# Kernel tuning notes

Measured on AMD Instinct MI355X. Metric: run time of the kernel, lower is better.

The kernel has to match this reference:

```python
import jax, jax.numpy as jnp
import numpy as np

D = 300  # feature dim hardcoded in the layer
L = 50   # headline length (e = ones(50))
B = 16384


def setup_inputs() -> dict:
    key = jax.random.key(0)
    ks = jax.random.split(key, 7)
    s = 0.05  # keras initializations.get('normal') uses scale=0.05
    return {
        "Y": jax.random.normal(ks[0], (B, D, L), dtype=jnp.float32),
        "h_n": jax.random.normal(ks[1], (B, D), dtype=jnp.float32),
        "W_y": s * jax.random.normal(ks[2], (D, D), dtype=jnp.float32),
        "W_h": s * jax.random.normal(ks[3], (D, D), dtype=jnp.float32),
        "W_p": s * jax.random.normal(ks[4], (D, D), dtype=jnp.float32),
        "W_x": s * jax.random.normal(ks[5], (D, D), dtype=jnp.float32),
        "w": s * jax.random.normal(ks[6], (D,), dtype=jnp.float32),
    }


def reference(Y, h_n, W_y, W_h, W_p, W_x, w):
    # M = tanh(W_y Y + (W_h h_n) e^T)   -> [B, D, L]
    Wh_h = jnp.einsum('de,be->bd', W_h, h_n)            # [B, D]
    M = jnp.tanh(jnp.einsum('de,bel->bdl', W_y, Y) + Wh_h[:, :, None])
    # alpha = softmax(w^T M) over headline positions    -> [B, L]
    alpha = jax.nn.softmax(jnp.einsum('d,bdl->bl', w, M), axis=-1)
    # r = Y alpha^T                                      -> [B, D]
    r = jnp.einsum('bdl,bl->bd', Y, alpha)
    # h* = tanh(W_p r + W_x h_n)                         -> [B, D]
    h = jnp.tanh(jnp.einsum('de,be->bd', W_p, r) + jnp.einsum('de,be->bd', W_x, h_n))
    return h
```

## Files before the change

### kernel.cpp

```cpp
#include <hip/hip_runtime.h>
#include <hip/hip_bf16.h>

typedef __attribute__((ext_vector_type(8))) short bf16x8;
typedef __attribute__((ext_vector_type(4))) float f32x4;
typedef unsigned short u16;
typedef unsigned int u32;

__device__ __forceinline__ u16 f2bf(float f){
    u32 u; __builtin_memcpy(&u,&f,4);
    u = (u + 0x7FFFu + ((u>>16)&1u)) >> 16;
    return (u16)u;
}
__device__ __forceinline__ float bf2f(u16 h){
    u32 u = ((u32)h)<<16; float f; __builtin_memcpy(&f,&u,4); return f;
}
__device__ __forceinline__ u32 pkbf(float a, float b){
    __hip_bfloat162 h = __float22bfloat162_rn(float2{a,b});
    u32 r; __builtin_memcpy(&r,&h,4); return r;
}
__device__ __forceinline__ float fast_tanh(float x){
    float e = __builtin_amdgcn_exp2f(x * 2.8853900817779268f);
    return 1.f - 2.f*__builtin_amdgcn_rcpf(e + 1.f);
}
__device__ __forceinline__ float wval(const float* W, int d, int e){
    return (d<300 && e<300) ? W[d*300+e] : 0.f;
}
__device__ __forceinline__ int yslot(int row){
    return (((row&15) ^ ((row>>2)&3) ^ ((row&48)>>2))) << 4;
}

__global__ void k_prep(const float* __restrict__ Wy, const float* __restrict__ Wh,
                       const float* __restrict__ Wp, const float* __restrict__ Wx,
                       const float* __restrict__ w,
                       u16* __restrict__ wy_swz, u16* __restrict__ wh_swz,
                       u16* __restrict__ wpx_swz, float* __restrict__ w_pad)
{
    int gid = blockIdx.x*256 + threadIdx.x;
    if (gid < 320) w_pad[gid] = (gid < 300) ? w[gid] : 0.f;
    u16* dst; const float* A; const float* Bm = nullptr; int t, nks;
    if (gid < 12800)      { dst = wy_swz;  t = gid;        nks = 10; A = Wy; }
    else if (gid < 25600) { dst = wh_swz;  t = gid-12800;  nks = 10; A = Wh; }
    else                  { dst = wpx_swz; t = gid-25600;  nks = 20; A = Wp; Bm = Wx; }
    int ks   = (t/64) % nks;
    int tile = t/(nks*64);
    int lane = t & 63;
    int d  = tile*16 + (lane & 15);
    int kb = ks*32 + (lane>>4)*8;
    u32 pk[4];
    #pragma unroll
    for (int jj=0; jj<4; jj++){
        int k0 = kb + 2*jj, k1 = k0 + 1;
        float v0, v1;
        if (Bm){ v0 = (k0 < 320) ? wval(A,d,k0) : wval(Bm,d,k0-320);
                 v1 = (k1 < 320) ? wval(A,d,k1) : wval(Bm,d,k1-320); }
        else   { v0 = wval(A,d,k0); v1 = wval(A,d,k1); }
        pk[jj] = (u32)f2bf(v0) | ((u32)f2bf(v1) << 16);
    }
    uint4 u; u.x = pk[0]; u.y = pk[1]; u.z = pk[2]; u.w = pk[3];
    ((uint4*)dst)[t] = u;
}

__global__ __launch_bounds__(256,3) void k_whh(const float* __restrict__ hn,
        const u16* __restrict__ wh_swz, u16* __restrict__ whh)
{
    __shared__ __align__(16) u16 A[64*328];
    int tid = threadIdx.x;
    int rb = blockIdx.x >> 1, half = blockIdx.x & 1;
    int m0 = rb*64;
    for (int i = tid; i < 9600; i += 256){
        int r = i/150, c = (i%150)*2;
        float2 v = *(const float2*)(hn + (size_t)(m0+r)*300 + c);
        *(u32*)&A[r*328 + c] = pkbf(v.x, v.y);
    }
    for (int i = tid; i < 64*14; i += 256){ int r = i/14, c = 300 + (i%14)*2; *(u32*)&A[r*328+c] = 0; }
    __syncthreads();
    int w = tid>>6, lane = tid&63, lo = lane&15, hi = lane>>4;
    f32x4 acc[10];
    #pragma unroll
    for (int t=0; t<10; t++) acc[t] = (f32x4){0.f,0.f,0.f,0.f};
    const bf16x8* wsz = (const bf16x8*)wh_swz;
    for (int ks=0; ks<10; ks++){
        bf16x8 aF = *(const bf16x8*)&A[(w*16+lo)*328 + ks*32 + hi*8];
        #pragma unroll
        for (int t=0; t<10; t++){
            int nt = half*10 + t;
            bf16x8 bF = wsz[(nt*10+ks)*64 + lane];
            acc[t] = __builtin_amdgcn_mfma_f32_16x16x32_bf16(aF, bF, acc[t], 0,0,0);
        }
    }
    #pragma unroll
    for (int t=0; t<10; t++)
      #pragma unroll
      for (int rg=0; rg<4; rg++){
        int m = m0 + w*16 + hi*4 + rg;
        whh[(size_t)m*320 + (half*10+t)*16 + lo] = f2bf(acc[t][rg]);
      }
}

__global__ __launch_bounds__(256,3) void k_attn(const float* __restrict__ Y,
        const u16* __restrict__ whh, const u16* __restrict__ wy_swz,
        const float* __restrict__ w_pad, u16* __restrict__ r_out)
{
    __shared__ __align__(16) u16 Ylds[64*384];
    __shared__ float whh_s[320];
    __shared__ float w_s[320];
    __shared__ float s_red[4][64];
    __shared__ float alpha_s[64];
    char* Yb8 = (char*)Ylds;
    int tid = threadIdx.x;
    int b = blockIdx.x;
    int w = tid>>6, lane = tid&63, lo = lane&15, hi = lane>>4;
    const float* Yb = Y + (size_t)b*15000;
    const float C2L = 2.8853900817779268f;

    #pragma unroll
    for (int it=0; it<7; it++){
        int t = tid + it*256;
        int e2 = t/12, l4 = (t%12)*4;
        const float* pA = Yb + e2*100 + l4;
        float4 a  = *(const float4*)pA;
        float2 b0 = *(const float2*)(pA + 50);
        float2 b1 = *(const float2*)(pA + 52);
        float av[4] = {a.x, a.y, a.z, a.w};
        float bv[4] = {b0.x, b0.y, b1.x, b1.y};
        #pragma unroll
        for (int j=0; j<4; j++){
            int row = l4 + j;
            *(u32*)(Yb8 + row*768 + ((e2*4) ^ yslot(row))) = pkbf(av[j], bv[j]);
        }
    }
    for (int t = tid + 1792; t < 1800; t += 256){
        int e2 = t/12, l4 = (t%12)*4;
        const float* pA = Yb + e2*100 + l4;
        float4 a  = *(const float4*)pA;
        float2 b0 = *(const float2*)(pA + 50);
        float2 b1 = *(const float2*)(pA + 52);
        float av[4] = {a.x, a.y, a.z, a.w};
        float bv[4] = {b0.x, b0.y, b1.x, b1.y};
        #pragma unroll
        for (int j=0; j<4; j++){
            int row = l4 + j;
            *(u32*)(Yb8 + row*768 + ((e2*4) ^ yslot(row))) = pkbf(av[j], bv[j]);
        }
    }
    if (tid < 150){
        int e2 = tid;
        float2 a = *(const float2*)(Yb + e2*100 + 48);
        float2 c = *(const float2*)(Yb + e2*100 + 98);
        *(u32*)(Yb8 + 48*768 + ((e2*4) ^ yslot(48))) = pkbf(a.x, c.x);
        *(u32*)(Yb8 + 49*768 + ((e2*4) ^ yslot(49))) = pkbf(a.y, c.y);
    }
    for (int i = tid; i < 500; i += 256){
        int row = i/10, e2 = 150 + i%10;
        *(u32*)(Yb8 + row*768 + ((e2*4) ^ yslot(row))) = 0;
    }
    for (int i = tid; i < 160; i += 256){
        u32 z = *(const u32*)&whh[(size_t)b*320 + 2*i];
        whh_s[2*i]   = bf2f((u16)(z & 0xffff));
        whh_s[2*i+1] = bf2f((u16)(z >> 16));
    }
    for (int i = tid; i < 320; i += 256) w_s[i] = w_pad[i];
    __syncthreads();

    const bf16x8* wyf = (const bf16x8*)wy_swz;
    float sp[4] = {0.f,0.f,0.f,0.f};
    float swd = 0.f;
    int rb_[4], sl_[4];
    #pragma unroll
    for (int c=0;c<4;c++){ int row=c*16+lo; rb_[c]=row*768; sl_[c]=yslot(row); }
    int hi16 = hi*16;

#define GEMM_PASS(Q0, NQ)                                                      \
    {                                                                          \
        f32x4 acc[NQ][4];                                                      \
        _Pragma("unroll") for (int q=0;q<NQ;q++)                               \
            _Pragma("unroll") for (int c=0;c<4;c++)                            \
                acc[q][c] = (f32x4){0.f,0.f,0.f,0.f};                          \
        bf16x8 A0[NQ], A1[NQ], B0[4], B1[4];                                   \
        _Pragma("unroll") for (int q=0;q<NQ;q++)                               \
            A0[q] = wyf[((w+4*((Q0)+q))*10)*64 + lane];                        \
        _Pragma("unroll") for (int c=0;c<4;c++)                                \
            B0[c] = *(const bf16x8*)(Yb8 + rb_[c] + (hi16 ^ sl_[c]));          \
        _Pragma("unroll 1")                                                    \
        for (int kk=0; kk<5; kk++){                                            \
            int k1 = 2*kk+1, k2 = 2*kk+2;                                      \
            int k2c = (k2 < 10) ? k2 : 0;                                      \
            _Pragma("unroll") for (int q=0;q<NQ;q++)                           \
                A1[q] = wyf[((w+4*((Q0)+q))*10 + k1)*64 + lane];               \
            _Pragma("unroll") for (int c=0;c<4;c++)                            \
                B1[c] = *(const bf16x8*)(Yb8 + rb_[c] + ((k1*64+hi16) ^ sl_[c])); \
            _Pragma("unroll") for (int q=0;q<NQ;q++)                           \
                _Pragma("unroll") for (int c=0;c<4;c++)                        \
                    acc[q][c] = __builtin_amdgcn_mfma_f32_16x16x32_bf16(       \
                        A0[q], B0[c], acc[q][c], 0,0,0);                       \
            _Pragma("unroll") for (int q=0;q<NQ;q++)                           \
                A0[q] = wyf[((w+4*((Q0)+q))*10 + k2)*64 + lane];               \
            _Pragma("unroll") for (int c=0;c<4;c++)                            \
                B0[c] = *(const bf16x8*)(Yb8 + rb_[c] + ((k2c*64+hi16) ^ sl_[c])); \
            _Pragma("unroll") for (int q=0;q<NQ;q++)                           \
                _Pragma("unroll") for (int c=0;c<4;c++)                        \
                    acc[q][c] = __builtin_amdgcn_mfma_f32_16x16x32_bf16(       \
                        A1[q], B1[c], acc[q][c], 0,0,0);                       \
        }                                                                      \
        _Pragma("unroll") for (int q=0;q<NQ;q++)                               \
            _Pragma("unroll") for (int rg=0;rg<4;rg++){                        \
                int d = (w + 4*((Q0)+q))*16 + hi*4 + rg;                       \
                float wh = whh_s[d], wd_ = w_s[d];                             \
                float whc = wh*C2L, wd2n = -2.f*wd_;                           \
                swd += wd_;                                                    \
                _Pragma("unroll") for (int c=0;c<4;c++){                       \
                    float targ = __builtin_fmaf(acc[q][c][rg], C2L, whc);      \
                    float e2x  = __builtin_amdgcn_exp2f(targ);                 \
                    float rc   = __builtin_amdgcn_rcpf(e2x + 1.f);             \
                    sp[c] = __builtin_fmaf(wd2n, rc, sp[c]);                   \
                }                                                              \
            }                                                                  \
    }

    GEMM_PASS(0, 3)
    GEMM_PASS(3, 2)
#undef GEMM_PASS

    #pragma unroll
    for (int c=0;c<4;c++){
        sp[c] += swd;
        sp[c] += __shfl_xor(sp[c], 16);
        sp[c] += __shfl_xor(sp[c], 32);
    }
    if (lane < 16){
        #pragma unroll
        for (int c=0;c<4;c++) s_red[w][c*16 + lane] = sp[c];
    }
    __syncthreads();

    if (w == 0){
        float sv = (lane < 50)
            ? (s_red[0][lane] + s_red[1][lane] + s_red[2][lane] + s_red[3][lane])
            : -1e30f;
        float mx = sv;
        #pragma unroll
        for (int off=32; off; off>>=1) mx = fmaxf(mx, __shfl_xor(mx, off));
        float pv = (lane < 50) ? __builtin_amdgcn_exp2f((sv - mx)*1.4426950408889634f) : 0.f;
        float sm = pv;
        #pragma unroll
        for (int off=32; off; off>>=1) sm += __shfl_xor(sm, off);
        alpha_s[lane] = pv * __builtin_amdgcn_rcpf(sm);
    }
    __syncthreads();

    if (tid < 160){
        float r0 = 0.f, r1 = 0.f;
        if (tid < 150){
            #pragma unroll 10
            for (int l=0; l<50; l++){
                u32 z = *(const u32*)(Yb8 + l*768 + ((tid*4) ^ yslot(l)));
                float a_ = alpha_s[l];
                r0 += a_ * bf2f((u16)(z & 0xffff));
                r1 += a_ * bf2f((u16)(z >> 16));
            }
        }
        *(u32*)&r_out[(size_t)b*320 + 2*tid] = pkbf(r0, r1);
    }
}

__global__ __launch_bounds__(256,3) void k_out(const u16* __restrict__ r_in,
        const float* __restrict__ hn, const u16* __restrict__ wpx_swz,
        float* __restrict__ out)
{
    __shared__ __align__(16) u16 A[32*648];
    int tid = threadIdx.x;
    int m0 = blockIdx.x*32;
    for (int i = tid; i < 32*40; i += 256){
        int r = i/40, c8 = (i%40)*8;
        uint4 v = *(const uint4*)&r_in[(size_t)(m0+r)*320 + c8];
        *(uint4*)&A[r*648 + c8] = v;
    }
    for (int i = tid; i < 32*150; i += 256){
        int r = i/150, c = (i%150)*2;
        float2 v = *(const float2*)(hn + (size_t)(m0+r)*300 + c);
        *(u32*)&A[r*648 + 320 + c] = pkbf(v.x, v.y);
    }
    for (int i = tid; i < 32*14; i += 256){ int r = i/14, c = 620 + (i%14)*2; *(u32*)&A[r*648+c] = 0; }
    __syncthreads();
    int w = tid>>6, lane = tid&63, lo = lane&15, hi = lane>>4;
    int wm = w & 1, wn = w >> 1;
    f32x4 acc[10];
    #pragma unroll
    for (int t=0; t<10; t++) acc[t] = (f32x4){0.f,0.f,0.f,0.f};
    const bf16x8* wsz = (const bf16x8*)wpx_swz;
    for (int ks=0; ks<20; ks++){
        bf16x8 aF = *(const bf16x8*)&A[(wm*16+lo)*648 + ks*32 + hi*8];
        #pragma unroll
        for (int t=0; t<10; t++){
            int nt = wn*10 + t;
            bf16x8 bF = wsz[(nt*20+ks)*64 + lane];
            acc[t] = __builtin_amdgcn_mfma_f32_16x16x32_bf16(aF, bF, acc[t], 0,0,0);
        }
    }
    #pragma unroll
    for (int t=0; t<10; t++){
        int n = (wn*10+t)*16 + lo;
        if (n < 300){
            #pragma unroll
            for (int rg=0; rg<4; rg++){
                int m = m0 + wm*16 + hi*4 + rg;
                out[(size_t)m*300 + n] = fast_tanh(acc[t][rg]);
            }
        }
    }
}

extern "C" void kernel_launch(void* const* d_in, const int* in_sizes, int n_in,
                              void* d_out, int out_size, void* d_ws, size_t ws_size,
                              hipStream_t stream)
{
    const float* Y  = (const float*)d_in[0];
    const float* hn = (const float*)d_in[1];
    const float* Wy = (const float*)d_in[2];
    const float* Wh = (const float*)d_in[3];
    const float* Wp = (const float*)d_in[4];
    const float* Wx = (const float*)d_in[5];
    const float* w  = (const float*)d_in[6];
    int B = in_sizes[1] / 300;

    char* ws = (char*)d_ws;
    u16*   wy_swz  = (u16*)(ws + 0);
    u16*   wh_swz  = (u16*)(ws + 204800);
    u16*   wpx_swz = (u16*)(ws + 409600);
    float* w_pad   = (float*)(ws + 819200);
    u16*   whh     = (u16*)(ws + 820480);
    u16*   r_ws    = (u16*)(ws + 820480 + (size_t)B*640);

    k_prep<<<200, 256, 0, stream>>>(Wy, Wh, Wp, Wx, w, wy_swz, wh_swz, wpx_swz, w_pad);
    k_whh <<<(B/64)*2, 256, 0, stream>>>(hn, wh_swz, whh);
    k_attn<<<B, 256, 0, stream>>>(Y, whh, wy_swz, w_pad, r_ws);
    k_out <<<B/32, 256, 0, stream>>>(r_ws, hn, wpx_swz, (float*)d_out);
}
```

Measured before the change: 494.5 us.

## Shrink Y LDS tile to padded 50-row layout to raise attention occupancy

Replaces the 64-row, 768-byte-stride XOR-swizzled Y tile in LDS with a 50-row tile padded to a 656-byte stride, dropping the swizzle. Rows 50-63 that the MFMA needs are aliased back onto existing rows, and staging now writes 8-byte chunks covering four features per task. The smaller LDS footprint lets launch_bounds go from 3 to 4 blocks per CU, with the aim of more latency hiding in this memory-bound kernel. The risk is more LDS bank conflicts from the padded stride compared with the swizzle, and extra register pressure under the tighter bound.

After: 507.4 us. +2.6%, slower.

```diff
diff --git a/kernel.cpp b/kernel.cpp
--- a/kernel.cpp
+++ b/kernel.cpp
@@ -24,9 +24,6 @@
 }
 __device__ __forceinline__ float wval(const float* W, int d, int e){
     return (d<300 && e<300) ? W[d*300+e] : 0.f;
-}
-__device__ __forceinline__ int yslot(int row){
-    return (((row&15) ^ ((row>>2)&3) ^ ((row&48)>>2))) << 4;
 }
 
 __global__ void k_prep(const float* __restrict__ Wy, const float* __restrict__ Wh,
@@ -97,11 +94,11 @@
       }
 }
 
-__global__ __launch_bounds__(256,3) void k_attn(const float* __restrict__ Y,
+__global__ __launch_bounds__(256,4) void k_attn(const float* __restrict__ Y,
         const u16* __restrict__ whh, const u16* __restrict__ wy_swz,
         const float* __restrict__ w_pad, u16* __restrict__ r_out)
 {
-    __shared__ __align__(16) u16 Ylds[64*384];
+    __shared__ __align__(16) u16 Ylds[50*328];
     __shared__ float whh_s[320];
     __shared__ float w_s[320];
     __shared__ float s_red[4][64];
@@ -113,46 +110,46 @@
     const float* Yb = Y + (size_t)b*15000;
     const float C2L = 2.8853900817779268f;
 
-    #pragma unroll
-    for (int it=0; it<7; it++){
-        int t = tid + it*256;
-        int e2 = t/12, l4 = (t%12)*4;
-        const float* pA = Yb + e2*100 + l4;
-        float4 a  = *(const float4*)pA;
-        float2 b0 = *(const float2*)(pA + 50);
-        float2 b1 = *(const float2*)(pA + 52);
-        float av[4] = {a.x, a.y, a.z, a.w};
-        float bv[4] = {b0.x, b0.y, b1.x, b1.y};
-        #pragma unroll
-        for (int j=0; j<4; j++){
-            int row = l4 + j;
-            *(u32*)(Yb8 + row*768 + ((e2*4) ^ yslot(row))) = pkbf(av[j], bv[j]);
-        }
-    }
-    for (int t = tid + 1792; t < 1800; t += 256){
-        int e2 = t/12, l4 = (t%12)*4;
-        const float* pA = Yb + e2*100 + l4;
-        float4 a  = *(const float4*)pA;
-        float2 b0 = *(const float2*)(pA + 50);
-        float2 b1 = *(const float2*)(pA + 52);
-        float av[4] = {a.x, a.y, a.z, a.w};
-        float bv[4] = {b0.x, b0.y, b1.x, b1.y};
-        #pragma unroll
-        for (int j=0; j<4; j++){
-            int row = l4 + j;
-            *(u32*)(Yb8 + row*768 + ((e2*4) ^ yslot(row))) = pkbf(av[j], bv[j]);
-        }
-    }
-    if (tid < 150){
-        int e2 = tid;
-        float2 a = *(const float2*)(Yb + e2*100 + 48);
-        float2 c = *(const float2*)(Yb + e2*100 + 98);
-        *(u32*)(Yb8 + 48*768 + ((e2*4) ^ yslot(48))) = pkbf(a.x, c.x);
-        *(u32*)(Yb8 + 49*768 + ((e2*4) ^ yslot(49))) = pkbf(a.y, c.y);
-    }
-    for (int i = tid; i < 500; i += 256){
-        int row = i/10, e2 = 150 + i%10;
-        *(u32*)(Yb8 + row*768 + ((e2*4) ^ yslot(row))) = 0;
+#define STAGE_TASK(T) do{                                                     \
+        int e4 = (T)/12, l4 = ((T)%12)*4;                                     \
+        const float* p0 = Yb + e4*200 + l4;                                   \
+        float4 r0 = *(const float4*)p0;                                       \
+        float2 r1a = *(const float2*)(p0+50), r1b = *(const float2*)(p0+52);  \
+        float4 r2 = *(const float4*)(p0+100);                                 \
+        float2 r3a = *(const float2*)(p0+150), r3b = *(const float2*)(p0+152);\
+        float e0v[4]={r0.x,r0.y,r0.z,r0.w};                                   \
+        float e1v[4]={r1a.x,r1a.y,r1b.x,r1b.y};                               \
+        float e2v[4]={r2.x,r2.y,r2.z,r2.w};                                   \
+        float e3v[4]={r3a.x,r3a.y,r3b.x,r3b.y};                               \
+        _Pragma("unroll")                                                     \
+        for (int j=0;j<4;j++){                                                \
+            int row = l4+j;                                                   \
+            uint2 uu; uu.x = pkbf(e0v[j], e1v[j]); uu.y = pkbf(e2v[j], e3v[j]);\
+            *(uint2*)(Yb8 + row*656 + e4*8) = uu;                             \
+        } }while(0)
+
+    {
+        #pragma unroll
+        for (int it=0; it<3; it++){ int t = tid + it*256; STAGE_TASK(t); }
+        if (tid < 132){ int t = tid + 768; STAGE_TASK(t); }
+    }
+#undef STAGE_TASK
+    if (tid < 75){
+        int e4 = tid;
+        const float* p0 = Yb + e4*200;
+        float2 a0 = *(const float2*)(p0+48);
+        float2 a1 = *(const float2*)(p0+98);
+        float2 a2 = *(const float2*)(p0+148);
+        float2 a3 = *(const float2*)(p0+198);
+        uint2 u48; u48.x = pkbf(a0.x, a1.x); u48.y = pkbf(a2.x, a3.x);
+        uint2 u49; u49.x = pkbf(a0.y, a1.y); u49.y = pkbf(a2.y, a3.y);
+        *(uint2*)(Yb8 + 48*656 + e4*8) = u48;
+        *(uint2*)(Yb8 + 49*656 + e4*8) = u49;
+    }
+    if (tid < 250){
+        int row = tid/5, q = tid%5;
+        uint2 z; z.x = 0; z.y = 0;
+        *(uint2*)(Yb8 + row*656 + 600 + q*8) = z;
     }
     for (int i = tid; i < 160; i += 256){
         u32 z = *(const u32*)&whh[(size_t)b*320 + 2*i];
@@ -165,9 +162,9 @@
     const bf16x8* wyf = (const bf16x8*)wy_swz;
     float sp[4] = {0.f,0.f,0.f,0.f};
     float swd = 0.f;
-    int rb_[4], sl_[4];
-    #pragma unroll
-    for (int c=0;c<4;c++){ int row=c*16+lo; rb_[c]=row*768; sl_[c]=yslot(row); }
+    int rb_[4];
+    #pragma unroll
+    for (int c=0;c<4;c++){ int row=c*16+lo; if (row>=50) row-=48; rb_[c]=row*656; }
     int hi16 = hi*16;
 
 #define GEMM_PASS(Q0, NQ)                                                      \
@@ -180,7 +177,7 @@
         _Pragma("unroll") for (int q=0;q<NQ;q++)                               \
             A0[q] = wyf[((w+4*((Q0)+q))*10)*64 + lane];                        \
         _Pragma("unroll") for (int c=0;c<4;c++)                                \
-            B0[c] = *(const bf16x8*)(Yb8 + rb_[c] + (hi16 ^ sl_[c]));          \
+            B0[c] = *(const bf16x8*)(Yb8 + rb_[c] + hi16);                     \
         _Pragma("unroll 1")                                                    \
         for (int kk=0; kk<5; kk++){                                            \
             int k1 = 2*kk+1, k2 = 2*kk+2;                                      \
@@ -188,7 +185,7 @@
             _Pragma("unroll") for (int q=0;q<NQ;q++)                           \
                 A1[q] = wyf[((w+4*((Q0)+q))*10 + k1)*64 + lane];               \
             _Pragma("unroll") for (int c=0;c<4;c++)                            \
-                B1[c] = *(const bf16x8*)(Yb8 + rb_[c] + ((k1*64+hi16) ^ sl_[c])); \
+                B1[c] = *(const bf16x8*)(Yb8 + rb_[c] + k1*64 + hi16);         \
             _Pragma("unroll") for (int q=0;q<NQ;q++)                           \
                 _Pragma("unroll") for (int c=0;c<4;c++)                        \
                     acc[q][c] = __builtin_amdgcn_mfma_f32_16x16x32_bf16(       \
@@ -196,7 +193,7 @@
             _Pragma("unroll") for (int q=0;q<NQ;q++)                           \
                 A0[q] = wyf[((w+4*((Q0)+q))*10 + k2)*64 + lane];               \
             _Pragma("unroll") for (int c=0;c<4;c++)                            \
-                B0[c] = *(const bf16x8*)(Yb8 + rb_[c] + ((k2c*64+hi16) ^ sl_[c])); \
+                B0[c] = *(const bf16x8*)(Yb8 + rb_[c] + k2c*64 + hi16);        \
             _Pragma("unroll") for (int q=0;q<NQ;q++)                           \
                 _Pragma("unroll") for (int c=0;c<4;c++)                        \
                     acc[q][c] = __builtin_amdgcn_mfma_f32_16x16x32_bf16(       \
@@ -253,7 +250,7 @@
         if (tid < 150){
             #pragma unroll 10
             for (int l=0; l<50; l++){
-                u32 z = *(const u32*)(Yb8 + l*768 + ((tid*4) ^ yslot(l)));
+                u32 z = *(const u32*)(Yb8 + l*656 + tid*4);
                 float a_ = alpha_s[l];
                 r0 += a_ * bf2f((u16)(z & 0xffff));
                 r1 += a_ * bf2f((u16)(z >> 16));
```
